# Optimization experiments

Hardware: AMD Instinct MI355X
Metric: run time of the kernel (lower is better)

## Reference

```python
import jax, jax.numpy as jnp
import numpy as np

N, D_IN, D_OUT, H, E = 8192, 1024, 1024, 1024, 8
EPS = 0.2
S_FACTOR = 5.0


def setup_inputs() -> dict:
    key = jax.random.key(0)
    k0, k1, k2, k3 = jax.random.split(key, 4)
    x = jax.random.normal(k0, (N, D_IN), jnp.float32)
    # selector Linear(nIn, E); weights scaled by sFactor as in SMoE.__init__
    Wsel = jax.random.normal(k1, (D_IN, E), jnp.float32) * (S_FACTOR / np.sqrt(D_IN))
    bsel = jnp.zeros((E,), jnp.float32)
    # stacked 2-layer MLP experts: Linear(D_IN,H) -> ReLU -> Linear(H,D_OUT)
    W1 = jax.random.normal(k2, (E, D_IN, H), jnp.float32) / np.sqrt(D_IN)
    b1 = jnp.zeros((E, H), jnp.float32)
    W2 = jax.random.normal(k3, (E, H, D_OUT), jnp.float32) / np.sqrt(H)
    b2 = jnp.zeros((E, D_OUT), jnp.float32)
    return {"x": x, "Wsel": Wsel, "bsel": bsel, "W1": W1, "b1": b1, "W2": W2, "b2": b2}


def _sparse_weights(weightMat):
    # sort experts per token, descending (torch.sort(..., 1, descending=True))
    order = jnp.argsort(-weightMat, axis=1)                # [N,E]
    topW = jnp.take_along_axis(weightMat, order, axis=1)
    cumW = jnp.cumsum(topW, axis=1)
    capped = jnp.minimum(cumW, 1.0 - EPS)
    sw_sorted = jax.nn.relu(capped - cumW + topW)          # sparse weights, sorted order
    # softCost (side-effect metric in the original; not returned by SMoE.forward)
    shifted = jnp.pad(sw_sorted[:, 1:], ((0, 0), (0, 1)))
    _soft_cost = jnp.sum(jnp.where(shifted > 0, 1.0, sw_sorted), axis=1)
    # faithful to torch.gather(sparse_weight, 1, index) in the source
    sw = jnp.take_along_axis(sw_sorted, order, axis=1)     # [N,E]
    return sw


def reference(x, Wsel, bsel, W1, b1, W2, b2):
    weightMat = jax.nn.softmax(x @ Wsel + bsel, axis=1)    # [N,E] selector
    sw = _sparse_weights(weightMat)                        # [N,E] sparse combine weights
    # dense (vectorized) expert dispatch: tokens with sw==0 contribute 0,
    # numerically identical to the gather/scatter_add loop in sparse_MoE
    h = jax.nn.relu(jnp.einsum('nd,edh->enh', x, W1) + b1[:, None, :])   # [E,N,H]
    y = jnp.einsum('enh,eho->eno', h, W2) + b2[:, None, :]               # [E,N,O]
    out = jnp.einsum('ne,eno->no', sw, y)                                # [N,O]
    return out
```

## Files before the change

kernel.cpp:

```cpp
#include <hip/hip_runtime.h>
#include <hip/hip_bf16.h>
#include <stdint.h>

#define N_TOK 8192
#define DIN   1024
#define DOUT  1024
#define HID   1024
#define NE    8
#define CAP   0.8f

typedef __attribute__((ext_vector_type(8))) short short8;
typedef __attribute__((ext_vector_type(4))) float floatx4;

__device__ __forceinline__ void async_load16(const void* g, void* l) {
  __builtin_amdgcn_global_load_lds(
      (const __attribute__((address_space(1))) void*)g,
      (__attribute__((address_space(3))) void*)l,
      16, 0, 0);
}

__device__ __forceinline__ unsigned short bf16_bits(float f) {
  return __builtin_bit_cast(unsigned short, __float2bfloat16(f));
}

__global__ __launch_bounds__(256) void zero_kernel(float4* __restrict__ out4, int n4) {
  const int stride = gridDim.x * 256;
  for (int i = blockIdx.x * 256 + threadIdx.x; i < n4; i += stride)
    out4[i] = (float4){0.f, 0.f, 0.f, 0.f};
}

__global__ __launch_bounds__(256) void selector_kernel(
    const float* __restrict__ x, const float* __restrict__ Wsel,
    const float* __restrict__ bsel,
    __hip_bfloat16* __restrict__ x_bf, float* __restrict__ sw)
{
  const int lane = threadIdx.x & 63;
  const int wave = threadIdx.x >> 6;
  const int n = blockIdx.x * 4 + wave;
  const float4* xr4 = (const float4*)(x + (size_t)n * DIN);
  ushort4* xb4 = (ushort4*)(x_bf + (size_t)n * DIN);

  float acc[8];
#pragma unroll
  for (int e = 0; e < 8; e++) acc[e] = 0.f;

#pragma unroll
  for (int i = 0; i < 4; i++) {
    const int d4 = lane + i * 64;
    const float4 xv = xr4[d4];
    ushort4 p;
    p.x = bf16_bits(xv.x);
    p.y = bf16_bits(xv.y);
    p.z = bf16_bits(xv.z);
    p.w = bf16_bits(xv.w);
    xb4[d4] = p;
    const float xs[4] = {xv.x, xv.y, xv.z, xv.w};
#pragma unroll
    for (int q = 0; q < 4; q++) {
      const int d = d4 * 4 + q;
      const float4* wr = (const float4*)(Wsel + d * 8);
      const float4 wlo = wr[0], whi = wr[1];
      const float xv1 = xs[q];
      acc[0] += xv1 * wlo.x; acc[1] += xv1 * wlo.y;
      acc[2] += xv1 * wlo.z; acc[3] += xv1 * wlo.w;
      acc[4] += xv1 * whi.x; acc[5] += xv1 * whi.y;
      acc[6] += xv1 * whi.z; acc[7] += xv1 * whi.w;
    }
  }
#pragma unroll
  for (int off = 32; off >= 1; off >>= 1)
#pragma unroll
    for (int e = 0; e < 8; e++) acc[e] += __shfl_xor(acc[e], off);

  if (lane == 0) {
    float w[8];
    float mx = -1e30f;
#pragma unroll
    for (int e = 0; e < 8; e++) { w[e] = acc[e] + bsel[e]; mx = fmaxf(mx, w[e]); }
    float s = 0.f;
#pragma unroll
    for (int e = 0; e < 8; e++) { w[e] = expf(w[e] - mx); s += w[e]; }
    const float inv = 1.f / s;
#pragma unroll
    for (int e = 0; e < 8; e++) w[e] *= inv;

    float wsrt[8]; int ord[8];
    for (int k = 0; k < 8; k++) {
      const float v = w[k];
      int j = k;
      while (j > 0 && wsrt[j - 1] < v) { wsrt[j] = wsrt[j - 1]; ord[j] = ord[j - 1]; j--; }
      wsrt[j] = v; ord[j] = k;
    }
    float cum = 0.f, sws[8];
    for (int k = 0; k < 8; k++) {
      cum += wsrt[k];
      const float capped = fminf(cum, CAP);
      sws[k] = fmaxf(capped - cum + wsrt[k], 0.f);
    }
    for (int j = 0; j < 8; j++) sw[(size_t)n * 8 + j] = sws[ord[j]];
  }
}

__global__ __launch_bounds__(1024) void compact_kernel(
    const float* __restrict__ sw, int* __restrict__ idx, int* __restrict__ cnt)
{
  const int e = blockIdx.x;
  const int t = threadIdx.x;
  const int lane = t & 63;
  const int wv = t >> 6;
  __shared__ int wave_base[16];
  __shared__ int chunk_total;
  int base = 0;
#pragma unroll
  for (int c = 0; c < 8; c++) {
    const int tok = c * 1024 + t;
    const bool act = sw[(size_t)tok * 8 + e] > 0.f;
    const unsigned long long m = __ballot(act);
    const int before = __popcll(m & ((1ull << lane) - 1ull));
    if (lane == 0) wave_base[wv] = __popcll(m);
    __syncthreads();
    if (t == 0) {
      int s = 0;
      for (int w = 0; w < 16; w++) { const int v = wave_base[w]; wave_base[w] = s; s += v; }
      chunk_total = s;
    }
    __syncthreads();
    if (act) idx[e * N_TOK + base + wave_base[wv] + before] = tok;
    base += chunk_total;
    __syncthreads();
  }
  if (t == 0) cnt[e] = base;
}

__global__ __launch_bounds__(256) void convert_weights_kernel(
    const float* __restrict__ W1, const float* __restrict__ W2,
    __hip_bfloat16* __restrict__ W1t, __hip_bfloat16* __restrict__ W2t)
{
  __shared__ float tile[32][33];
  const int z = blockIdx.z;
  const float* src = (z & 8) ? W2 : W1;
  __hip_bfloat16* dst = (z & 8) ? W2t : W1t;
  const int e = z & 7;
  src += (size_t)e * 1024 * 1024;
  dst += (size_t)e * 1024 * 1024;
  const int R = blockIdx.y * 32, C = blockIdx.x * 32;
  const int c = threadIdx.x & 31, r0 = threadIdx.x >> 5;
#pragma unroll
  for (int p = 0; p < 4; p++) {
    const int r = r0 + p * 8;
    tile[r][c] = src[(size_t)(R + r) * 1024 + C + c];
  }
  __syncthreads();
#pragma unroll
  for (int p = 0; p < 4; p++) {
    const int r = r0 + p * 8;
    dst[(size_t)(C + r) * 1024 + R + c] = __float2bfloat16(tile[c][r]);
  }
}

template <int MODE>
__global__ __launch_bounds__(256, 2) void moe_gemm(
    const __hip_bfloat16* __restrict__ x_bf,
    __hip_bfloat16* __restrict__ hpool,
    const __hip_bfloat16* __restrict__ Wt,
    const float* __restrict__ biasAll,
    const float* __restrict__ sw,
    const int* __restrict__ idx, const int* __restrict__ cnt,
    float* __restrict__ out)
{
  const int e = blockIdx.z;
  const int count = cnt[e];
  const int m0 = blockIdx.y * 128;
  if (m0 >= count) return;
  const int n0 = blockIdx.x * 128;

  __shared__ __align__(16) __hip_bfloat16 sA[128 * 32];
  __shared__ __align__(16) __hip_bfloat16 sB[128 * 32];
  const int t = threadIdx.x;
  const int lane = t & 63;
  const int wave = t >> 6;
  const int wm = (wave & 1) * 64;
  const int wn = (wave >> 1) * 64;
  const int* idx_e = idx + e * N_TOK;
  const float* bias = biasAll + e * 1024;

  floatx4 acc[4][4];
#pragma unroll
  for (int i = 0; i < 4; i++)
#pragma unroll
    for (int j = 0; j < 4; j++) acc[i][j] = (floatx4){0.f, 0.f, 0.f, 0.f};

  const int sr = t >> 2;
  const int sc = (t & 3) * 8;
  const __hip_bfloat16* Ag0;
  const __hip_bfloat16* Ag1;
  if (MODE == 0) {
    const int t0 = idx_e[min(m0 + sr, count - 1)];
    const int t1 = idx_e[min(m0 + sr + 64, count - 1)];
    Ag0 = x_bf + (size_t)t0 * 1024 + sc;
    Ag1 = x_bf + (size_t)t1 * 1024 + sc;
  } else {
    const __hip_bfloat16* hp = hpool + (size_t)e * N_TOK * 1024;
    Ag0 = hp + (size_t)(m0 + sr) * 1024 + sc;
    Ag1 = hp + (size_t)(m0 + sr + 64) * 1024 + sc;
  }
  const __hip_bfloat16* Bg = Wt + (size_t)e * 1024 * 1024 + (size_t)(n0 + sr) * 1024 + sc;
  __hip_bfloat16* lA = &sA[sr * 32 + sc];
  __hip_bfloat16* lB = &sB[sr * 32 + sc];

  const int rf = lane & 15;
  const int k8 = (lane >> 4) * 8;
  const __hip_bfloat16* sAr = &sA[(wm + rf) * 32 + k8];
  const __hip_bfloat16* sBr = &sB[(wn + rf) * 32 + k8];

  for (int k0 = 0; k0 < 1024; k0 += 32) {
    async_load16(Ag0 + k0, lA);
    async_load16(Ag1 + k0, lA + 64 * 32);
    async_load16(Bg + k0, lB);
    async_load16(Bg + (size_t)64 * 1024 + k0, lB + 64 * 32);
    __syncthreads();
    short8 aF[4], bF[4];
#pragma unroll
    for (int i = 0; i < 4; i++) aF[i] = *(const short8*)(sAr + i * 16 * 32);
#pragma unroll
    for (int j = 0; j < 4; j++) bF[j] = *(const short8*)(sBr + j * 16 * 32);
#pragma unroll
    for (int i = 0; i < 4; i++)
#pragma unroll
      for (int j = 0; j < 4; j++)
        acc[i][j] = __builtin_amdgcn_mfma_f32_16x16x32_bf16(aF[i], bF[j], acc[i][j], 0, 0, 0);
    __syncthreads();
  }

  const int quad = lane >> 4;
  const int cn = lane & 15;
#pragma unroll
  for (int i = 0; i < 4; i++) {
#pragma unroll
    for (int r = 0; r < 4; r++) {
      const int gm = m0 + wm + i * 16 + quad * 4 + r;
      if (gm >= count) continue;
      int tok = 0; float swv = 0.f;
      if (MODE == 1) {
        tok = idx_e[gm];
        swv = sw[tok * 8 + e];
      }
#pragma unroll
      for (int j = 0; j < 4; j++) {
        const int gn = n0 + wn + j * 16 + cn;
        const float v = acc[i][j][r] + bias[gn];
        if (MODE == 0) {
          hpool[((size_t)e * N_TOK + gm) * 1024 + gn] = __float2bfloat16(fmaxf(v, 0.f));
        } else {
          unsafeAtomicAdd(&out[(size_t)tok * 1024 + gn], swv * v);
        }
      }
    }
  }
}

extern "C" void kernel_launch(void* const* d_in, const int* in_sizes, int n_in,
                              void* d_out, int out_size, void* d_ws, size_t ws_size,
                              hipStream_t stream) {
  const float* x    = (const float*)d_in[0];
  const float* Wsel = (const float*)d_in[1];
  const float* bsel = (const float*)d_in[2];
  const float* W1   = (const float*)d_in[3];
  const float* b1   = (const float*)d_in[4];
  const float* W2   = (const float*)d_in[5];
  const float* b2   = (const float*)d_in[6];
  float* out = (float*)d_out;

  char* ws = (char*)d_ws;
  __hip_bfloat16* x_bf = (__hip_bfloat16*)ws; ws += (size_t)N_TOK * DIN * 2;
  __hip_bfloat16* W1t  = (__hip_bfloat16*)ws; ws += (size_t)NE * DIN * HID * 2;
  __hip_bfloat16* W2t  = (__hip_bfloat16*)ws; ws += (size_t)NE * HID * DOUT * 2;
  float* sw            = (float*)ws;          ws += (size_t)N_TOK * NE * 4;
  int* idx             = (int*)ws;            ws += (size_t)NE * N_TOK * 4;
  int* cnt             = (int*)ws;            ws += 256;
  __hip_bfloat16* hpool = (__hip_bfloat16*)ws;

  zero_kernel<<<1024, 256, 0, stream>>>((float4*)out, N_TOK * DOUT / 4);
  selector_kernel<<<N_TOK / 4, 256, 0, stream>>>(x, Wsel, bsel, x_bf, sw);
  compact_kernel<<<NE, 1024, 0, stream>>>(sw, idx, cnt);
  convert_weights_kernel<<<dim3(32, 32, 16), 256, 0, stream>>>(W1, W2, W1t, W2t);

  moe_gemm<0><<<dim3(HID / 128, N_TOK / 128, NE), 256, 0, stream>>>(
      x_bf, hpool, W1t, b1, sw, idx, cnt, out);
  moe_gemm<1><<<dim3(DOUT / 128, N_TOK / 128, NE), 256, 0, stream>>>(
      x_bf, hpool, W2t, b2, sw, idx, cnt, out);
}
```

Before: 321.8 us.

## Double-buffer LDS tiles in MoE GEMM to overlap loads with MFMA

Allocates two LDS buffers for the A and B tiles and issues the async global-to-LDS loads for the next K slice before computing on the current one. This cuts the barrier count per K step from two to one. The aim is to hide global load latency behind the MFMA work. It doubles LDS use per block, which could affect occupancy, and relies on the barrier waiting for outstanding async loads.

Measured after the change: 321.9 us. No clear change (+0.0%).

```diff
diff --git a/kernel.cpp b/kernel.cpp
--- a/kernel.cpp
+++ b/kernel.cpp
@@ -157,6 +157,8 @@
     dst[(size_t)(C + r) * 1024 + R + c] = __float2bfloat16(tile[c][r]);
   }
 }
+
+#define BUFO (128 * 32)
 
 template <int MODE>
 __global__ __launch_bounds__(256, 2) void moe_gemm(
@@ -174,8 +176,8 @@
   if (m0 >= count) return;
   const int n0 = blockIdx.x * 128;
 
-  __shared__ __align__(16) __hip_bfloat16 sA[128 * 32];
-  __shared__ __align__(16) __hip_bfloat16 sB[128 * 32];
+  __shared__ __align__(16) __hip_bfloat16 sA[2 * BUFO];
+  __shared__ __align__(16) __hip_bfloat16 sB[2 * BUFO];
   const int t = threadIdx.x;
   const int lane = t & 63;
   const int wave = t >> 6;
@@ -210,27 +212,45 @@
 
   const int rf = lane & 15;
   const int k8 = (lane >> 4) * 8;
-  const __hip_bfloat16* sAr = &sA[(wm + rf) * 32 + k8];
-  const __hip_bfloat16* sBr = &sB[(wn + rf) * 32 + k8];
-
-  for (int k0 = 0; k0 < 1024; k0 += 32) {
-    async_load16(Ag0 + k0, lA);
-    async_load16(Ag1 + k0, lA + 64 * 32);
-    async_load16(Bg + k0, lB);
-    async_load16(Bg + (size_t)64 * 1024 + k0, lB + 64 * 32);
-    __syncthreads();
-    short8 aF[4], bF[4];
-#pragma unroll
-    for (int i = 0; i < 4; i++) aF[i] = *(const short8*)(sAr + i * 16 * 32);
-#pragma unroll
-    for (int j = 0; j < 4; j++) bF[j] = *(const short8*)(sBr + j * 16 * 32);
-#pragma unroll
-    for (int i = 0; i < 4; i++)
-#pragma unroll
-      for (int j = 0; j < 4; j++)
-        acc[i][j] = __builtin_amdgcn_mfma_f32_16x16x32_bf16(aF[i], bF[j], acc[i][j], 0, 0, 0);
-    __syncthreads();
-  }
+  const int roA = (wm + rf) * 32 + k8;
+  const int roB = (wn + rf) * 32 + k8;
+
+  async_load16(Ag0, lA);
+  async_load16(Ag1, lA + 64 * 32);
+  async_load16(Bg, lB);
+  async_load16(Bg + (size_t)64 * 1024, lB + 64 * 32);
+  __syncthreads();
+
+#define STEP(KT, RB, WB)                                                        \
+  {                                                                             \
+    const int knext = ((KT) + 1) * 32;                                          \
+    if (knext < 1024) {                                                         \
+      async_load16(Ag0 + knext, lA + (WB) * BUFO);                              \
+      async_load16(Ag1 + knext, lA + (WB) * BUFO + 64 * 32);                    \
+      async_load16(Bg + knext, lB + (WB) * BUFO);                               \
+      async_load16(Bg + (size_t)64 * 1024 + knext, lB + (WB) * BUFO + 64 * 32); \
+    }                                                                           \
+    const __hip_bfloat16* pA = &sA[(RB) * BUFO + roA];                          \
+    const __hip_bfloat16* pB = &sB[(RB) * BUFO + roB];                          \
+    short8 aF[4], bF[4];                                                        \
+    _Pragma("unroll")                                                           \
+    for (int i = 0; i < 4; i++) aF[i] = *(const short8*)(pA + i * 16 * 32);     \
+    _Pragma("unroll")                                                           \
+    for (int j = 0; j < 4; j++) bF[j] = *(const short8*)(pB + j * 16 * 32);     \
+    _Pragma("unroll")                                                           \
+    for (int i = 0; i < 4; i++)                                                 \
+      _Pragma("unroll")                                                         \
+      for (int j = 0; j < 4; j++)                                               \
+        acc[i][j] = __builtin_amdgcn_mfma_f32_16x16x32_bf16(aF[i], bF[j],       \
+                                                            acc[i][j], 0, 0, 0);\
+    __syncthreads();                                                            \
+  }
+
+  for (int kt = 0; kt < 32; kt += 2) {
+    STEP(kt, 0, 1);
+    STEP(kt + 1, 1, 0);
+  }
+#undef STEP
 
   const int quad = lane >> 4;
   const int cn = lane & 15;
```
